# Optimization experiments

Measured on AMD Instinct MI355X. Metric: run time of the kernel, lower is better.

The kernel has to match this reference:

```python
import jax, jax.numpy as jnp
import numpy as np


def setup_inputs() -> dict:
    key = jax.random.key(0)
    ks = jax.random.split(key, 8)
    B, T, D, H, HD = 4, 2048, 1024, 16, 64
    s = 0.02
    return {
        "x": jax.random.normal(ks[0], (B, T, D), dtype=jnp.float32),
        "Wq": jax.random.normal(ks[1], (H, D, HD), dtype=jnp.float32) * s,
        "bq": jnp.zeros((H, HD), dtype=jnp.float32),
        "Wk": jax.random.normal(ks[2], (H, D, HD), dtype=jnp.float32) * s,
        "bk": jnp.zeros((H, HD), dtype=jnp.float32),
        "Wv": jax.random.normal(ks[3], (H, D, HD), dtype=jnp.float32) * s,
        "bv": jnp.zeros((H, HD), dtype=jnp.float32),
        "Wo": jax.random.normal(ks[4], (D, D), dtype=jnp.float32) * s,
        "bo": jnp.zeros((D,), dtype=jnp.float32),
        "mask": 1,
    }


def reference(x, Wq, bq, Wk, bk, Wv, bv, Wo, bo, mask):
    B, T, D = x.shape
    # stacked per-head projections: [B,H,T,hd]
    q = jnp.einsum('btd,hde->bhte', x, Wq) + bq[None, :, None, :]
    k = jnp.einsum('btd,hde->bhte', x, Wk) + bk[None, :, None, :]
    v = jnp.einsum('btd,hde->bhte', x, Wv) + bv[None, :, None, :]
    hd = q.shape[-1]
    # FAITHFUL to source: scores = QK^T / hd**(-0.5) == QK^T * sqrt(hd)
    scores = jnp.einsum('bhte,bhse->bhts', q, k) * (float(hd) ** 0.5)
    if mask:
        causal = jnp.tril(jnp.ones((T, T), dtype=bool))
        scores = jnp.where(causal[None, None, :, :], scores, -jnp.inf)
    att = jax.nn.softmax(scores, axis=-1)  # dropout is identity in eval
    out = jnp.einsum('bhts,bhse->bhte', att, v)
    # concat heads along feature dim (head order matches ModuleList order)
    out = out.transpose(0, 2, 1, 3).reshape(B, T, D)
    return out @ Wo + bo
```

## Files before the change

### kernel.cpp

```cpp
#include <hip/hip_runtime.h>
#include <hip/hip_bf16.h>
#include <math.h>

#define B_  4
#define T_  2048
#define D_  1024
#define H_  16
#define HD_ 64
#define M_  8192

typedef __attribute__((ext_vector_type(8))) _Float16 f16x8;
typedef __attribute__((ext_vector_type(4))) float   f32x4;

static __device__ __forceinline__ unsigned short f2h(float f){
    union { _Float16 h; unsigned short u; } cv; cv.h = (_Float16)f; return cv.u;
}
static __device__ __forceinline__ void gload_lds16(const void* g, void* l){
    __builtin_amdgcn_global_load_lds(
        (const __attribute__((address_space(1))) unsigned int*)g,
        (__attribute__((address_space(3))) unsigned int*)l, 16, 0, 0);
}

union U16x16 { unsigned short us[16]; uint4 q[2]; };
union U16x4  { unsigned short us[4];  uint2 q;    };

__global__ __launch_bounds__(256) void prep_xh(
    const float* __restrict__ x, unsigned short* __restrict__ xb)
{
    const size_t i = ((size_t)blockIdx.x*256 + threadIdx.x)*16;
    U16x16 u;
#pragma unroll
    for (int j=0;j<16;j+=4){
        float4 f = *(const float4*)(x+i+j);
        u.us[j+0]=f2h(f.x); u.us[j+1]=f2h(f.y);
        u.us[j+2]=f2h(f.z); u.us[j+3]=f2h(f.w);
    }
    *(uint4*)(xb+i)   = u.q[0];
    *(uint4*)(xb+i+8) = u.q[1];
}

__global__ __launch_bounds__(256) void prep_wqkvh(
    const float* __restrict__ Wq, const float* __restrict__ Wk,
    const float* __restrict__ Wv, unsigned short* __restrict__ wt)
{
    const int dt = blockIdx.x;
    const int zh = blockIdx.y;
    const int z = zh >> 4, h = zh & 15;
    const float* src = ((z==0)?Wq:(z==1)?Wk:Wv) + (size_t)h*1024*64;
    __shared__ float Tt[64][68];
    const int t = threadIdx.x;
    const int r = t >> 2, c4 = (t & 3) * 16;
    const float* sp = src + (size_t)(dt*64 + r)*64 + c4;
    float4 v0=*(const float4*)(sp+0), v1=*(const float4*)(sp+4);
    float4 v2=*(const float4*)(sp+8), v3=*(const float4*)(sp+12);
    *(float4*)&Tt[r][c4+ 0]=v0; *(float4*)&Tt[r][c4+ 4]=v1;
    *(float4*)&Tt[r][c4+ 8]=v2; *(float4*)&Tt[r][c4+12]=v3;
    __syncthreads();
    const int er = t >> 2, dk = (t & 3) * 16;
    U16x16 u;
#pragma unroll
    for (int j=0;j<16;j++) u.us[j] = f2h(Tt[dk+j][er]);
    unsigned short* dst = wt + (size_t)(z*1024 + h*64 + er)*1024 + dt*64 + dk;
    *(uint4*)(dst)   = u.q[0];
    *(uint4*)(dst+8) = u.q[1];
}

__global__ __launch_bounds__(256) void prep_woh(
    const float* __restrict__ Wo, unsigned short* __restrict__ wot)
{
    const int kt = blockIdx.x, nt = blockIdx.y;
    __shared__ float Tt[64][68];
    const int t = threadIdx.x;
    const int r = t >> 2, c4 = (t & 3) * 16;
    const float* sp = Wo + (size_t)(kt*64 + r)*1024 + nt*64 + c4;
    float4 v0=*(const float4*)(sp+0), v1=*(const float4*)(sp+4);
    float4 v2=*(const float4*)(sp+8), v3=*(const float4*)(sp+12);
    *(float4*)&Tt[r][c4+ 0]=v0; *(float4*)&Tt[r][c4+ 4]=v1;
    *(float4*)&Tt[r][c4+ 8]=v2; *(float4*)&Tt[r][c4+12]=v3;
    __syncthreads();
    const int er = t >> 2, dk = (t & 3) * 16;
    U16x16 u;
#pragma unroll
    for (int j=0;j<16;j++) u.us[j] = f2h(Tt[dk+j][er]);
    unsigned short* dst = wot + (size_t)(nt*64 + er)*1024 + kt*64 + dk;
    *(uint4*)(dst)   = u.q[0];
    *(uint4*)(dst+8) = u.q[1];
}

__global__ __launch_bounds__(256) void gemm_qkvh(
    const unsigned short* __restrict__ xb, const unsigned short* __restrict__ wt,
    const float* __restrict__ bqv, const float* __restrict__ bkv,
    const float* __restrict__ bvv,
    unsigned short* __restrict__ qp, unsigned short* __restrict__ kp,
    unsigned short* __restrict__ vtp)
{
    const int m0 = blockIdx.x * 128;
    const int n0 = blockIdx.y * 128;
    const int tid = threadIdx.x;
    const int lane = tid & 63, w = tid >> 6;
    const int wr = w >> 1, wc = w & 1;
    const int fla = lane & 15, flb = lane >> 4;

    __shared__ unsigned short As[128*32];
    __shared__ unsigned short Bs[128*32];

    f32x4 acc[4][4];
#pragma unroll
    for (int i=0;i<4;i++)
#pragma unroll
        for (int j=0;j<4;j++) acc[i][j] = (f32x4){0.f,0.f,0.f,0.f};

    const int srow0 = w*32 + (lane>>2);
    const int srow1 = srow0 + 16;
    const int spc   = lane & 3;
    const size_t ga0 = (size_t)(m0+srow0)*1024 + (size_t)((spc ^ ((srow0>>1)&3))*8);
    const size_t ga1 = (size_t)(m0+srow1)*1024 + (size_t)((spc ^ ((srow1>>1)&3))*8);
    const size_t gb0 = (size_t)(n0+srow0)*1024 + (size_t)((spc ^ ((srow0>>1)&3))*8);
    const size_t gb1 = (size_t)(n0+srow1)*1024 + (size_t)((spc ^ ((srow1>>1)&3))*8);
    const int ldso0 = w*1024;
    const int ldso1 = w*1024 + 512;
    const int pchunk = (flb ^ ((fla>>1)&3)) * 8;

    for (int ks = 0; ks < 32; ++ks){
        const size_t k0 = (size_t)ks*32;
        __syncthreads();
        gload_lds16(xb + ga0 + k0, As + ldso0);
        gload_lds16(xb + ga1 + k0, As + ldso1);
        gload_lds16(wt + gb0 + k0, Bs + ldso0);
        gload_lds16(wt + gb1 + k0, Bs + ldso1);
        __syncthreads();

        f16x8 af[4], bfr[4];
#pragma unroll
        for (int mf=0; mf<4; ++mf)
            af[mf] = *(const f16x8*)&As[(wr*64+mf*16+fla)*32 + pchunk];
#pragma unroll
        for (int nf=0; nf<4; ++nf)
            bfr[nf] = *(const f16x8*)&Bs[(wc*64+nf*16+fla)*32 + pchunk];
#pragma unroll
        for (int mf=0; mf<4; ++mf)
#pragma unroll
            for (int nf=0; nf<4; ++nf)
                acc[mf][nf] = __builtin_amdgcn_mfma_f32_16x16x32_f16(
                                  af[mf], bfr[nf], acc[mf][nf], 0, 0, 0);
    }

#pragma unroll
    for (int nf=0; nf<4; ++nf){
        const int c = n0 + wc*64 + nf*16 + fla;
        const int z = c >> 10, rem = c & 1023;
        const int h = rem >> 6, e = rem & 63;
        if (z < 2){
            const float bias = ((z==0)?bqv:bkv)[rem];
            const float scl  = (z==0) ? 11.541560327111708f
                                      : 1.0f;
            unsigned short* op = (z==0)?qp:kp;
#pragma unroll
            for (int mf=0; mf<4; ++mf){
#pragma unroll
                for (int ri=0; ri<4; ++ri){
                    const int m = m0 + wr*64 + mf*16 + flb*4 + ri;
                    const int b = m >> 11, t = m & (T_-1);
                    op[((size_t)(b*H_ + h)*T_ + t)*HD_ + e] =
                        f2h((acc[mf][nf][ri] + bias) * scl);
                }
            }
        } else {
            const float bias = bvv[rem];
#pragma unroll
            for (int mf=0; mf<4; ++mf){
                const int m = m0 + wr*64 + mf*16 + flb*4;
                const int b = m >> 11, t = m & (T_-1);
                U16x4 u;
#pragma unroll
                for (int ri=0; ri<4; ++ri)
                    u.us[ri] = f2h(acc[mf][nf][ri] + bias);
                *(uint2*)(vtp + ((size_t)(b*H_ + h)*HD_ + e)*T_ + t) = u.q;
            }
        }
    }
}

__global__ __launch_bounds__(256) void gemm_o(
    const unsigned short* __restrict__ attb, const unsigned short* __restrict__ wot,
    const float* __restrict__ bo, float* __restrict__ out)
{
    const int m0 = blockIdx.x * 128;
    const int n0 = blockIdx.y * 128;
    const int tid = threadIdx.x;
    const int lane = tid & 63, w = tid >> 6;
    const int wr = w >> 1, wc = w & 1;
    const int fla = lane & 15, flb = lane >> 4;

    __shared__ unsigned short As[4096];
    __shared__ unsigned short Bs[4096];

    f32x4 acc[4][4];
#pragma unroll
    for (int i=0;i<4;i++)
#pragma unroll
        for (int j=0;j<4;j++) acc[i][j] = (f32x4){0.f,0.f,0.f,0.f};

    const int srow0 = w*32 + (lane>>2);
    const int srow1 = srow0 + 16;
    const int spc   = lane & 3;
    const size_t ga0 = (size_t)(m0+srow0)*1024 + (size_t)((spc ^ ((srow0>>1)&3))*8);
    const size_t ga1 = (size_t)(m0+srow1)*1024 + (size_t)((spc ^ ((srow1>>1)&3))*8);
    const size_t gb0 = (size_t)(n0+srow0)*1024 + (size_t)((spc ^ ((srow0>>1)&3))*8);
    const size_t gb1 = (size_t)(n0+srow1)*1024 + (size_t)((spc ^ ((srow1>>1)&3))*8);
    const int ldso0 = w*1024;
    const int ldso1 = w*1024 + 512;
    const int pchunk = (flb ^ ((fla>>1)&3)) * 8;

    for (int ks = 0; ks < 32; ++ks){
        const size_t k0 = (size_t)ks*32;
        __syncthreads();
        gload_lds16(attb + ga0 + k0, As + ldso0);
        gload_lds16(attb + ga1 + k0, As + ldso1);
        gload_lds16(wot  + gb0 + k0, Bs + ldso0);
        gload_lds16(wot  + gb1 + k0, Bs + ldso1);
        __syncthreads();

        f16x8 af[4], bfr[4];
#pragma unroll
        for (int mf=0; mf<4; ++mf)
            af[mf] = *(const f16x8*)&As[(wr*64+mf*16+fla)*32 + pchunk];
#pragma unroll
        for (int nf=0; nf<4; ++nf)
            bfr[nf] = *(const f16x8*)&Bs[(wc*64+nf*16+fla)*32 + pchunk];
#pragma unroll
        for (int mf=0; mf<4; ++mf)
#pragma unroll
            for (int nf=0; nf<4; ++nf)
                acc[mf][nf] = __builtin_amdgcn_mfma_f32_16x16x32_f16(
                                  af[mf], bfr[nf], acc[mf][nf], 0, 0, 0);
    }

#pragma unroll
    for (int nf=0; nf<4; ++nf){
        const int n = n0 + wc*64 + nf*16 + fla;
        const float bias = bo[n];
#pragma unroll
        for (int mf=0; mf<4; ++mf){
#pragma unroll
            for (int ri=0; ri<4; ++ri){
                const int m = m0 + wr*64 + mf*16 + flb*4 + ri;
                out[(size_t)m*D_ + n] = acc[mf][nf][ri] + bias;
            }
        }
    }
}

__global__ __launch_bounds__(256) void attn_mfma(
    const unsigned short* __restrict__ qp, const unsigned short* __restrict__ kp,
    const unsigned short* __restrict__ vtp, unsigned short* __restrict__ attb,
    const int* __restrict__ maskp)
{
    const int bid = blockIdx.x;
    const int qb  = 31 - (bid >> 6);
    const int bh  = bid & 63;
    const int b   = bh >> 4, h = bh & 15;
    const int tid = threadIdx.x;
    const int lane = tid & 63, w = tid >> 6;
    const int l16 = lane & 15, h16 = lane >> 4;
    const int domask = maskp[0];

    __shared__ unsigned short KS [2][64][32];
    __shared__ unsigned short VtS[2][64][32];
    __shared__ unsigned short PsS[2][64][32];

    const int qrow = qb*64 + w*16 + l16;
    const size_t qoff = ((size_t)bh*T_ + qrow)*HD_ + 8*h16;
    const f16x8 q0 = *(const f16x8*)(qp + qoff);
    const f16x8 q1 = *(const f16x8*)(qp + qoff + 32);

    f32x4 accO[4];
#pragma unroll
    for (int j=0;j<4;j++) accO[j] = (f32x4){0.f,0.f,0.f,0.f};
    float m_run[4], l_run[4];
#pragma unroll
    for (int i=0;i<4;i++){ m_run[i] = -INFINITY; l_run[i] = 0.f; }

    const int r   = tid >> 2;
    const int cq  = tid & 3;
    const int sci = cq >> 1;
    const int sb0 = (cq & 1) * 2;
    const int fr  = (r >> 1) & 3;
    const int sd0 = ((sb0  ) ^ fr)*8;
    const int sd1 = ((sb0+1) ^ fr)*8;
    const int c16 = cq * 16;

    const int off = (h16 ^ ((l16>>1)&3)) * 8;

    const size_t kbase = (size_t)bh*T_*HD_;
    const size_t vbase = (size_t)bh*HD_*T_;

    const int kv_end = domask ? qb : 31;
    for (int kv = 0; kv <= kv_end; ++kv){
        const unsigned short* ksrc = kp + kbase + (size_t)(kv*64+r)*HD_ + c16;
        uint4 a0 = *(const uint4*)(ksrc);
        uint4 a1 = *(const uint4*)(ksrc+8);
        const unsigned short* vsrc = vtp + vbase + (size_t)r*T_ + kv*64 + c16;
        uint4 a4 = *(const uint4*)(vsrc);
        uint4 a5 = *(const uint4*)(vsrc+8);
        __syncthreads();
        *(uint4*)&KS [sci][r][sd0] = a0; *(uint4*)&KS [sci][r][sd1] = a1;
        *(uint4*)&VtS[sci][r][sd0] = a4; *(uint4*)&VtS[sci][r][sd1] = a5;
        __syncthreads();

        f32x4 s[4];
#pragma unroll
        for (int j=0;j<4;j++){
            const f16x8 k0 = *(const f16x8*)&KS[0][j*16+l16][off];
            const f16x8 k1 = *(const f16x8*)&KS[1][j*16+l16][off];
            f32x4 a = (f32x4){0.f,0.f,0.f,0.f};
            a = __builtin_amdgcn_mfma_f32_16x16x32_f16(q0, k0, a, 0,0,0);
            a = __builtin_amdgcn_mfma_f32_16x16x32_f16(q1, k1, a, 0,0,0);
            s[j] = a;
        }
        if (domask && kv == qb){
#pragma unroll
            for (int j=0;j<4;j++)
#pragma unroll
                for (int reg=0;reg<4;reg++)
                    if (j*16+l16 > w*16 + h16*4 + reg) s[j][reg] = -INFINITY;
        }

        float pmax[4];
#pragma unroll
        for (int reg=0; reg<4; ++reg){
            float mloc = fmaxf(fmaxf(s[0][reg],s[1][reg]), fmaxf(s[2][reg],s[3][reg]));
            mloc = fmaxf(mloc, __shfl_xor(mloc,1));
            mloc = fmaxf(mloc, __shfl_xor(mloc,2));
            mloc = fmaxf(mloc, __shfl_xor(mloc,4));
            mloc = fmaxf(mloc, __shfl_xor(mloc,8));
            pmax[reg] = mloc;
        }
        const bool small = (pmax[0] <= m_run[0]+8.f) && (pmax[1] <= m_run[1]+8.f)
                        && (pmax[2] <= m_run[2]+8.f) && (pmax[3] <= m_run[3]+8.f);
        if (!__all(small)){
#pragma unroll
            for (int reg=0; reg<4; ++reg){
                const float mnew = fmaxf(m_run[reg], pmax[reg]);
                const float scl  = exp2f(m_run[reg] - mnew);
                m_run[reg] = mnew;
                l_run[reg] *= scl;
                accO[0][reg] *= scl; accO[1][reg] *= scl;
                accO[2][reg] *= scl; accO[3][reg] *= scl;
            }
        }
        const int sbl = l16 >> 3, pos = l16 & 7;
#pragma unroll
        for (int reg=0; reg<4; ++reg){
            const float mr = m_run[reg];
            float p0 = exp2f(s[0][reg]-mr);
            float p1 = exp2f(s[1][reg]-mr);
            float p2 = exp2f(s[2][reg]-mr);
            float p3 = exp2f(s[3][reg]-mr);
            float rs = p0+p1+p2+p3;
            rs += __shfl_xor(rs,1); rs += __shfl_xor(rs,2);
            rs += __shfl_xor(rs,4); rs += __shfl_xor(rs,8);
            l_run[reg] += rs;
            const int prow = w*16 + h16*4 + reg;
            const int psw  = (prow>>1)&3;
            PsS[0][prow][((sbl  ) ^ psw)*8 + pos] = f2h(p0);
            PsS[0][prow][((sbl+2) ^ psw)*8 + pos] = f2h(p1);
            PsS[1][prow][((sbl  ) ^ psw)*8 + pos] = f2h(p2);
            PsS[1][prow][((sbl+2) ^ psw)*8 + pos] = f2h(p3);
        }

#pragma unroll
        for (int c=0;c<2;c++){
            const f16x8 pa = *(const f16x8*)&PsS[c][w*16+l16][off];
#pragma unroll
            for (int j=0;j<4;j++){
                const f16x8 vb_ = *(const f16x8*)&VtS[c][j*16+l16][off];
                accO[j] = __builtin_amdgcn_mfma_f32_16x16x32_f16(pa, vb_, accO[j], 0,0,0);
            }
        }
    }

#pragma unroll
    for (int reg=0;reg<4;reg++){
        const float inv = 1.0f / l_run[reg];
        const int t = qb*64 + w*16 + h16*4 + reg;
#pragma unroll
        for (int j=0;j<4;j++){
            attb[((size_t)b*T_ + t)*D_ + h*HD_ + j*16 + l16] =
                f2h(accO[j][reg]*inv);
        }
    }
}

extern "C" void kernel_launch(void* const* d_in, const int* in_sizes, int n_in,
                              void* d_out, int out_size, void* d_ws, size_t ws_size,
                              hipStream_t stream)
{
    const float* x  = (const float*)d_in[0];
    const float* Wq = (const float*)d_in[1];
    const float* bq = (const float*)d_in[2];
    const float* Wk = (const float*)d_in[3];
    const float* bk = (const float*)d_in[4];
    const float* Wv = (const float*)d_in[5];
    const float* bv = (const float*)d_in[6];
    const float* Wo = (const float*)d_in[7];
    const float* bo = (const float*)d_in[8];
    const int* mask = (const int*)d_in[9];
    float* out = (float*)d_out;

    unsigned short* qp  = (unsigned short*)d_ws;
    unsigned short* kp  = qp  + (size_t)8*1024*1024;
    unsigned short* vtp = kp  + (size_t)8*1024*1024;
    unsigned short* xb  = vtp + (size_t)8*1024*1024;
    unsigned short* wt  = xb  + (size_t)8*1024*1024;
    unsigned short* wot = wt  + (size_t)3*1024*1024;
    unsigned short* attb = xb;

    prep_xh   <<<2048, 256, 0, stream>>>(x, xb);
    prep_wqkvh<<<dim3(16,48), 256, 0, stream>>>(Wq, Wk, Wv, wt);
    prep_woh  <<<dim3(16,16), 256, 0, stream>>>(Wo, wot);
    gemm_qkvh <<<dim3(64,24), 256, 0, stream>>>(xb, wt, bq, bk, bv, qp, kp, vtp);
    attn_mfma <<<2048, 256, 0, stream>>>(qp, kp, vtp, attb, mask);
    gemm_o    <<<dim3(64,8), 256, 0, stream>>>(attb, wot, bo, out);
}
```

Measured before the change: 215.2 us.

## Process 128-key chunks per iteration and defer row-sum reduction to epilogue

The attention loop now stages 128 keys per iteration instead of 64, halving the number of barrier pairs and loop iterations, with causal masking applied on the final chunk using absolute positions. The per-row softmax sum is kept as a per-lane partial and reduced across lanes only once at the end, removing four shuffles per row per iteration. This doubles shared memory for K, V and P tiles and the score registers, and for odd query blocks the last chunk computes half-masked extra work.

```diff
diff --git a/kernel.cpp b/kernel.cpp
--- a/kernel.cpp
+++ b/kernel.cpp
@@ -265,9 +265,9 @@
     const int l16 = lane & 15, h16 = lane >> 4;
     const int domask = maskp[0];
 
-    __shared__ unsigned short KS [2][64][32];
-    __shared__ unsigned short VtS[2][64][32];
-    __shared__ unsigned short PsS[2][64][32];
+    __shared__ unsigned short KS [2][128][32];
+    __shared__ unsigned short VtS[4][64][32];
+    __shared__ unsigned short PsS[4][64][32];
 
     const int qrow = qb*64 + w*16 + l16;
     const size_t qoff = ((size_t)bh*T_ + qrow)*HD_ + 8*h16;
@@ -277,40 +277,45 @@
     f32x4 accO[4];
 #pragma unroll
     for (int j=0;j<4;j++) accO[j] = (f32x4){0.f,0.f,0.f,0.f};
-    float m_run[4], l_run[4];
-#pragma unroll
-    for (int i=0;i<4;i++){ m_run[i] = -INFINITY; l_run[i] = 0.f; }
-
-    const int r   = tid >> 2;
-    const int cq  = tid & 3;
-    const int sci = cq >> 1;
-    const int sb0 = (cq & 1) * 2;
-    const int fr  = (r >> 1) & 3;
-    const int sd0 = ((sb0  ) ^ fr)*8;
-    const int sd1 = ((sb0+1) ^ fr)*8;
-    const int c16 = cq * 16;
+    float m_run[4], lpart[4];
+#pragma unroll
+    for (int i=0;i<4;i++){ m_run[i] = -INFINITY; lpart[i] = 0.f; }
+
+    const int kr = tid >> 1;
+    const int kh = tid & 1;
+    const int fk = (kr >> 1) & 3;
+    const int vr = tid >> 2;
+    const int vq = tid & 3;
+    const int fv = (vr >> 1) & 3;
 
     const int off = (h16 ^ ((l16>>1)&3)) * 8;
 
     const size_t kbase = (size_t)bh*T_*HD_;
     const size_t vbase = (size_t)bh*HD_*T_;
 
-    const int kv_end = domask ? qb : 31;
-    for (int kv = 0; kv <= kv_end; ++kv){
-        const unsigned short* ksrc = kp + kbase + (size_t)(kv*64+r)*HD_ + c16;
-        uint4 a0 = *(const uint4*)(ksrc);
-        uint4 a1 = *(const uint4*)(ksrc+8);
-        const unsigned short* vsrc = vtp + vbase + (size_t)r*T_ + kv*64 + c16;
-        uint4 a4 = *(const uint4*)(vsrc);
-        uint4 a5 = *(const uint4*)(vsrc+8);
-        __syncthreads();
-        *(uint4*)&KS [sci][r][sd0] = a0; *(uint4*)&KS [sci][r][sd1] = a1;
-        *(uint4*)&VtS[sci][r][sd0] = a4; *(uint4*)&VtS[sci][r][sd1] = a5;
-        __syncthreads();
-
-        f32x4 s[4];
-#pragma unroll
-        for (int j=0;j<4;j++){
+    const int nchunks = domask ? ((qb+2)>>1) : 16;
+    for (int ci = 0; ci < nchunks; ++ci){
+        const int kb = ci << 7;
+        const unsigned short* ksrc = kp + kbase + (size_t)(kb+kr)*HD_ + kh*32;
+        uint4 ka0=*(const uint4*)(ksrc),    ka1=*(const uint4*)(ksrc+8);
+        uint4 ka2=*(const uint4*)(ksrc+16), ka3=*(const uint4*)(ksrc+24);
+        const unsigned short* vsrc = vtp + vbase + (size_t)vr*T_ + kb + vq*32;
+        uint4 va0=*(const uint4*)(vsrc),    va1=*(const uint4*)(vsrc+8);
+        uint4 va2=*(const uint4*)(vsrc+16), va3=*(const uint4*)(vsrc+24);
+        __syncthreads();
+        *(uint4*)&KS [kh][kr][(0^fk)*8] = ka0;
+        *(uint4*)&KS [kh][kr][(1^fk)*8] = ka1;
+        *(uint4*)&KS [kh][kr][(2^fk)*8] = ka2;
+        *(uint4*)&KS [kh][kr][(3^fk)*8] = ka3;
+        *(uint4*)&VtS[vq][vr][(0^fv)*8] = va0;
+        *(uint4*)&VtS[vq][vr][(1^fv)*8] = va1;
+        *(uint4*)&VtS[vq][vr][(2^fv)*8] = va2;
+        *(uint4*)&VtS[vq][vr][(3^fv)*8] = va3;
+        __syncthreads();
+
+        f32x4 s[8];
+#pragma unroll
+        for (int j=0;j<8;j++){
             const f16x8 k0 = *(const f16x8*)&KS[0][j*16+l16][off];
             const f16x8 k1 = *(const f16x8*)&KS[1][j*16+l16][off];
             f32x4 a = (f32x4){0.f,0.f,0.f,0.f};
@@ -318,18 +323,21 @@
             a = __builtin_amdgcn_mfma_f32_16x16x32_f16(q1, k1, a, 0,0,0);
             s[j] = a;
         }
-        if (domask && kv == qb){
-#pragma unroll
-            for (int j=0;j<4;j++)
+        if (domask && ci == nchunks-1){
+#pragma unroll
+            for (int j=0;j<8;j++)
 #pragma unroll
                 for (int reg=0;reg<4;reg++)
-                    if (j*16+l16 > w*16 + h16*4 + reg) s[j][reg] = -INFINITY;
+                    if (kb + j*16 + l16 > qb*64 + w*16 + h16*4 + reg)
+                        s[j][reg] = -INFINITY;
         }
 
         float pmax[4];
 #pragma unroll
         for (int reg=0; reg<4; ++reg){
-            float mloc = fmaxf(fmaxf(s[0][reg],s[1][reg]), fmaxf(s[2][reg],s[3][reg]));
+            float m0 = fmaxf(fmaxf(s[0][reg],s[1][reg]), fmaxf(s[2][reg],s[3][reg]));
+            float m1 = fmaxf(fmaxf(s[4][reg],s[5][reg]), fmaxf(s[6][reg],s[7][reg]));
+            float mloc = fmaxf(m0, m1);
             mloc = fmaxf(mloc, __shfl_xor(mloc,1));
             mloc = fmaxf(mloc, __shfl_xor(mloc,2));
             mloc = fmaxf(mloc, __shfl_xor(mloc,4));
@@ -344,37 +352,34 @@
                 const float mnew = fmaxf(m_run[reg], pmax[reg]);
                 const float scl  = exp2f(m_run[reg] - mnew);
                 m_run[reg] = mnew;
-                l_run[reg] *= scl;
+                lpart[reg] *= scl;
                 accO[0][reg] *= scl; accO[1][reg] *= scl;
                 accO[2][reg] *= scl; accO[3][reg] *= scl;
             }
         }
-        const int sbl = l16 >> 3, pos = l16 & 7;
+
+        const int sblo = l16 >> 3, pos = l16 & 7;
 #pragma unroll
         for (int reg=0; reg<4; ++reg){
             const float mr = m_run[reg];
-            float p0 = exp2f(s[0][reg]-mr);
-            float p1 = exp2f(s[1][reg]-mr);
-            float p2 = exp2f(s[2][reg]-mr);
-            float p3 = exp2f(s[3][reg]-mr);
-            float rs = p0+p1+p2+p3;
-            rs += __shfl_xor(rs,1); rs += __shfl_xor(rs,2);
-            rs += __shfl_xor(rs,4); rs += __shfl_xor(rs,8);
-            l_run[reg] += rs;
             const int prow = w*16 + h16*4 + reg;
             const int psw  = (prow>>1)&3;
-            PsS[0][prow][((sbl  ) ^ psw)*8 + pos] = f2h(p0);
-            PsS[0][prow][((sbl+2) ^ psw)*8 + pos] = f2h(p1);
-            PsS[1][prow][((sbl  ) ^ psw)*8 + pos] = f2h(p2);
-            PsS[1][prow][((sbl+2) ^ psw)*8 + pos] = f2h(p3);
-        }
-
-#pragma unroll
-        for (int c=0;c<2;c++){
-            const f16x8 pa = *(const f16x8*)&PsS[c][w*16+l16][off];
+            float ps = 0.f;
+#pragma unroll
+            for (int j=0;j<8;j++){
+                const float p = exp2f(s[j][reg]-mr);
+                ps += p;
+                PsS[j>>1][prow][(((j&1)*2 + sblo) ^ psw)*8 + pos] = f2h(p);
+            }
+            lpart[reg] += ps;
+        }
+
+#pragma unroll
+        for (int kc=0;kc<4;kc++){
+            const f16x8 pa = *(const f16x8*)&PsS[kc][w*16+l16][off];
 #pragma unroll
             for (int j=0;j<4;j++){
-                const f16x8 vb_ = *(const f16x8*)&VtS[c][j*16+l16][off];
+                const f16x8 vb_ = *(const f16x8*)&VtS[kc][j*16+l16][off];
                 accO[j] = __builtin_amdgcn_mfma_f32_16x16x32_f16(pa, vb_, accO[j], 0,0,0);
             }
         }
@@ -382,7 +387,10 @@
 
 #pragma unroll
     for (int reg=0;reg<4;reg++){
-        const float inv = 1.0f / l_run[reg];
+        float l = lpart[reg];
+        l += __shfl_xor(l,1); l += __shfl_xor(l,2);
+        l += __shfl_xor(l,4); l += __shfl_xor(l,8);
+        const float inv = 1.0f / l;
         const int t = qb*64 + w*16 + h16*4 + reg;
 #pragma unroll
         for (int j=0;j<4;j++){
```

Measured after the change: 203.4 us. -5.5%, faster.
